# Kernel tuning notes

Hardware: AMD Instinct MI355X
Metric: run time of the kernel (lower is better)

## Reference

```python
import jax, jax.numpy as jnp
import numpy as np

N, E, IN, H, D, C = 30000, 400000, 128, 4, 64, 40
EPS = 1e-5
SLOPE = 0.2  # DGL GATv2Conv leaky_relu negative_slope default


def setup_inputs() -> dict:
    key = jax.random.key(0)
    ks = jax.random.split(key, 20)
    def rn(k, shape, s=0.05):
        return jax.random.normal(k, shape, jnp.float32) * s
    return {
        "x": jax.random.normal(ks[0], (N, IN), jnp.float32),
        "src": jax.random.randint(ks[1], (E,), 0, N),
        "dst": jax.random.randint(ks[2], (E,), 0, N),
        # layer 0: in=128 -> heads*64 (residual projection since 128 != 256)
        "W_src0": rn(ks[3], (IN, H * D)), "W_dst0": rn(ks[4], (IN, H * D)),
        "b0": jnp.zeros((H * D,), jnp.float32), "attn0": rn(ks[5], (H, D)),
        "res_W0": rn(ks[6], (IN, H * D)),
        # layer 1: 256 -> heads*64 (identity residual since 256 == 256)
        "W_src1": rn(ks[7], (H * D, H * D)), "W_dst1": rn(ks[8], (H * D, H * D)),
        "b1": jnp.zeros((H * D,), jnp.float32), "attn1": rn(ks[9], (H, D)),
        # layer 2: 256 -> heads*40 (residual projection)
        "W_src2": rn(ks[10], (H * D, H * C)), "W_dst2": rn(ks[11], (H * D, H * C)),
        "b2": jnp.zeros((H * C,), jnp.float32), "attn2": rn(ks[12], (H, C)),
        "res_W2": rn(ks[13], (H * D, H * C)),
        # batchnorm affine params (training-mode batch stats)
        "g0": jnp.ones((H * D,), jnp.float32), "be0": jnp.zeros((H * D,), jnp.float32),
        "g1": jnp.ones((H * D,), jnp.float32), "be1": jnp.zeros((H * D,), jnp.float32),
    }


def gatv2_layer(h, src, dst, Wsrc, Wdst, b, attn, resW, out_dim, relu_act):
    # DGL GATv2Conv: score_e = attn . leaky_relu(fc_src(h)[u] + fc_dst(h)[v])
    n = h.shape[0]
    fs = (h @ Wsrc).reshape(n, H, out_dim)
    fd = (h @ Wdst).reshape(n, H, out_dim)
    e = jax.nn.leaky_relu(fs[src] + fd[dst], SLOPE)      # [E, H, out]
    score = jnp.einsum("ehd,hd->eh", e, attn)            # [E, H]
    # segment softmax over incoming edges of each dst node
    m = jax.ops.segment_max(score, dst, num_segments=n)
    m = jnp.where(jnp.isfinite(m), m, 0.0)               # zero in-degree safety
    ex = jnp.exp(score - m[dst])
    denom = jax.ops.segment_sum(ex, dst, num_segments=n)
    alpha = ex / jnp.maximum(denom, 1e-9)[dst]
    rst = jax.ops.segment_sum(alpha[:, :, None] * fs[src], dst, num_segments=n)
    res = (h @ resW).reshape(n, H, out_dim) if resW is not None else h.reshape(n, H, out_dim)
    rst = rst + res + b.reshape(1, H, out_dim)
    return jax.nn.relu(rst) if relu_act else rst


def batchnorm(h, g, be):
    mu = h.mean(0)
    var = h.var(0)  # biased variance, as torch BN uses for normalization
    return g * (h - mu) * jax.lax.rsqrt(var + EPS) + be


def reference(x, src, dst, W_src0, W_dst0, b0, attn0, res_W0, W_src1, W_dst1, b1, attn1, W_src2, W_dst2, b2, attn2, res_W2, g0, be0, g1, be1):
    h = gatv2_layer(x, src, dst, W_src0, W_dst0, b0, attn0, res_W0, D, True)
    h = jax.nn.relu(batchnorm(h.reshape(N, H * D), g0, be0))  # dropout = identity (eval)
    h = gatv2_layer(h, src, dst, W_src1, W_dst1, b1, attn1, None, D, True)
    h = jax.nn.relu(batchnorm(h.reshape(N, H * D), g1, be1))
    h = gatv2_layer(h, src, dst, W_src2, W_dst2, b2, attn2, res_W2, C, False)
    h = h.mean(1)  # mean over heads -> [N, C]
    return jax.nn.log_softmax(h, axis=-1)
```

## Files before the change

kernel.cpp:

```cpp
#include <hip/hip_runtime.h>
#include <hip/hip_bf16.h>
#include <math.h>

#define NN 30000
#define EE 400000
#define INP 128
#define HH 4
#define DD 64
#define CC 40
#define HD 256
#define HC 160
#define NBLK 118

typedef unsigned short ushort;
typedef __attribute__((ext_vector_type(8))) short s8v;
typedef __attribute__((ext_vector_type(4))) float f4v;
typedef __attribute__((ext_vector_type(2))) float f2;


__device__ inline ushort bf16_of_float(float f) {
    __hip_bfloat16 b = __float2bfloat16(f);
    return *(ushort*)&b;
}
__device__ __forceinline__ float b2f(ushort u) { return __uint_as_float(((unsigned)u) << 16); }

__device__ __forceinline__ f2 cvt2v(unsigned d) {
    f2 r;
    r.x = __uint_as_float(d << 16);
    r.y = __uint_as_float(d & 0xFFFF0000u);
    return r;
}
__device__ __forceinline__ f2 splat2(float s) { f2 r = {s, s}; return r; }
__device__ __forceinline__ f2 f2fmav(f2 a, f2 b, f2 c) {
#if __has_builtin(__builtin_elementwise_fma)
    return __builtin_elementwise_fma(a, b, c);
#else
    f2 r; r.x = __fmaf_rn(a.x, b.x, c.x); r.y = __fmaf_rn(a.y, b.y, c.y); return r;
#endif
}
__device__ __forceinline__ f2 f2maxv(f2 a, f2 b) {
#if __has_builtin(__builtin_elementwise_max)
    return __builtin_elementwise_max(a, b);
#else
    f2 r; r.x = fmaxf(a.x, b.x); r.y = fmaxf(a.y, b.y); return r;
#endif
}

__device__ __forceinline__ void gld16(const void* g, void* l) {
    __builtin_amdgcn_global_load_lds((const __attribute__((address_space(1))) void*)g,
                                     (__attribute__((address_space(3))) void*)l, 16, 0, 0);
}

__device__ __forceinline__ float rowsum16(float x) {
    int t;
    t = __builtin_amdgcn_update_dpp(0, __float_as_int(x), 0x128, 0xF, 0xF, false); x += __int_as_float(t);
    t = __builtin_amdgcn_update_dpp(0, __float_as_int(x), 0x124, 0xF, 0xF, false); x += __int_as_float(t);
    t = __builtin_amdgcn_update_dpp(0, __float_as_int(x), 0x122, 0xF, 0xF, false); x += __int_as_float(t);
    t = __builtin_amdgcn_update_dpp(0, __float_as_int(x), 0x121, 0xF, 0xF, false); x += __int_as_float(t);
    return x;
}
__device__ __forceinline__ float rowmax16(float x) {
    int t;
    t = __builtin_amdgcn_update_dpp(0, __float_as_int(x), 0x128, 0xF, 0xF, false); x = fmaxf(x, __int_as_float(t));
    t = __builtin_amdgcn_update_dpp(0, __float_as_int(x), 0x124, 0xF, 0xF, false); x = fmaxf(x, __int_as_float(t));
    t = __builtin_amdgcn_update_dpp(0, __float_as_int(x), 0x122, 0xF, 0xF, false); x = fmaxf(x, __int_as_float(t));
    t = __builtin_amdgcn_update_dpp(0, __float_as_int(x), 0x121, 0xF, 0xF, false); x = fmaxf(x, __int_as_float(t));
    return x;
}

#define XB 3750
#define TB 1408
#define ZB 240

__global__ __launch_bounds__(256) void k_prep(const float* __restrict__ x, ushort* __restrict__ xc,
        const float* W0, const float* W1, const float* W2, const float* W3,
        const float* W4, const float* W5, const float* W6, const float* W7,
        ushort* bt0, ushort* bt1, ushort* bt2,
        int* __restrict__ zero_region,
        const float* b0, const float* a0, const float* b1, const float* a1,
        const float* b2, const float* a2, const float* g0, const float* be0,
        const float* g1, const float* be1, ushort* __restrict__ smallv) {
    int b = blockIdx.x, t = threadIdx.x;
    if (b < XB) {
        int i = b * 256 + t;
        if (i < NN * INP / 4) {
            float4 v = ((const float4*)x)[i];
            ushort4 o;
            o.x = bf16_of_float(v.x); o.y = bf16_of_float(v.y);
            o.z = bf16_of_float(v.z); o.w = bf16_of_float(v.w);
            ((ushort4*)xc)[i] = o;
        }
    } else if (b < XB + TB) {
        const float* Ws[8] = {W0, W1, W2, W3, W4, W5, W6, W7};
        int g = (b - XB) * 256 + t;
        if (g < 98304) {
            int seg = g >> 15, local = g & 32767;
            int n = local >> 7, k = local & 127;
            bt0[g] = bf16_of_float(Ws[seg][k * 256 + n]);
        } else if (g < 229376) {
            int gg = g - 98304;
            int seg = gg >> 16, local = gg & 65535;
            int n = local >> 8, k = local & 255;
            bt1[gg] = bf16_of_float(Ws[3 + seg][k * 256 + n]);
        } else if (g < 360448) {
            int gg = g - 229376;
            int n = gg >> 8, k = gg & 255;
            ushort val = 0;
            if (n < 480) {
                int seg = n / 160;
                int nn = n - seg * 160;
                val = bf16_of_float(Ws[5 + seg][k * 160 + nn]);
            }
            bt2[gg] = val;
        }
    } else if (b < XB + TB + ZB) {
        int i = (b - XB - TB) * 256 + t;
        if (i < 1024 + 2 * NN + 192) zero_region[i] = 0;
    } else {
        const float* ptrs[10] = {b0, a0, b1, a1, b2, a2, g0, be0, g1, be1};
        const int sz[10] = {256, 256, 256, 256, 160, 160, 256, 256, 256, 256};
        int off = 0;
        for (int j = 0; j < 10; j++) {
            if (t < sz[j]) smallv[off + t] = bf16_of_float(ptrs[j][t]);
            off += sz[j];
        }
    }
}


__global__ __launch_bounds__(256) void k_hist(const int* __restrict__ dst, int* __restrict__ cnt) {
    int e = blockIdx.x * 256 + threadIdx.x;
    if (e < EE) atomicAdd(&cnt[dst[e]], 1);
}

__global__ __launch_bounds__(256) void k_binbeg(const int* __restrict__ cnt, int* __restrict__ binCnt,
                                                int* __restrict__ beg, int* __restrict__ total) {
    __shared__ int lb[64];
    __shared__ int ss[256];
    __shared__ int base;
    int t = threadIdx.x;
    if (t < 64) lb[t] = 0;
    __syncthreads();
    int i = blockIdx.x * 256 + t;
    int c = (i < NN) ? cnt[i] : 0;
    if (i < NN) atomicAdd(&lb[63 - min(c, 63)], 1);
    ss[t] = c;
    __syncthreads();
    if (t < 64 && lb[t] > 0) atomicAdd(&binCnt[t], lb[t]);
    for (int o = 1; o < 256; o <<= 1) {
        int v = (t >= o) ? ss[t - o] : 0;
        __syncthreads();
        ss[t] += v;
        __syncthreads();
    }
    if (t == 255) base = atomicAdd(total, ss[255]);
    __syncthreads();
    if (i < NN) beg[i] = base + ss[t] - c;
}

__global__ __launch_bounds__(256) void k_orderscatter(const int* __restrict__ cnt, const int* __restrict__ binCnt,
                                                      int* __restrict__ binPos, int* __restrict__ order,
                                                      const int* __restrict__ src, const int* __restrict__ dst,
                                                      const int* __restrict__ beg, int* __restrict__ pos,
                                                      int* __restrict__ srcs) {
    int t = threadIdx.x;
    if (blockIdx.x < NBLK) {
        __shared__ int lb[64], lbase[64], bpre[64];
        if (t < 64) { lb[t] = 0; bpre[t] = binCnt[t]; }
        __syncthreads();
        int i = blockIdx.x * 256 + t;
        int bin = 0, rank = 0;
        if (i < NN) {
            bin = 63 - min(cnt[i], 63);
            rank = atomicAdd(&lb[bin], 1);
        }
        for (int o = 1; o < 64; o <<= 1) {
            int v = (t >= o && t < 64) ? bpre[t - o] : 0;
            __syncthreads();
            if (t < 64) bpre[t] += v;
            __syncthreads();
        }
        if (t < 64 && lb[t] > 0)
            lbase[t] = bpre[t] - binCnt[t] + atomicAdd(&binPos[t], lb[t]);
        __syncthreads();
        if (i < NN) order[lbase[bin] + rank] = i;
    } else {
        int e = (blockIdx.x - NBLK) * 256 + t;
        if (e < EE) {
            int d = dst[e];
            int p = atomicAdd(&pos[d], 1);
            srcs[beg[d] + p] = src[e];
        }
    }
}


template<int K, int SEGW, int NSEG>
__global__ __launch_bounds__(256) void k_gemm_tiled(const ushort* __restrict__ A,
                                                    const ushort* __restrict__ Bt,
                                                    ushort* __restrict__ o0, ushort* __restrict__ o1,
                                                    ushort* __restrict__ o2) {
    __shared__ ushort As[2 * 128 * 32];
    __shared__ ushort Bs[2 * 128 * 32];
    int t = threadIdx.x;
    int wave = t >> 6, lane = t & 63;
    int m = lane & 15, q = lane >> 4;
    int row0 = blockIdx.x * 128, col0 = blockIdx.y * 128;
    int wr = (wave >> 1) << 6, wc = (wave & 1) << 6;
    f4v acc[4][4] = {};
    int c1 = t, c2 = t + 256;
    int ar1 = min(row0 + (c1 >> 2), NN - 1);
    int ar2 = min(row0 + (c2 >> 2), NN - 1);
    const ushort* a1 = A + (size_t)ar1 * K + (c1 & 3) * 8;
    const ushort* a2 = A + (size_t)ar2 * K + (c2 & 3) * 8;
    const ushort* b1 = Bt + (size_t)(col0 + (c1 >> 2)) * K + (c1 & 3) * 8;
    const ushort* b2 = Bt + (size_t)(col0 + (c2 >> 2)) * K + (c2 & 3) * 8;
    int wbase = wave << 10;
    char* AsB = (char*)As;
    char* BsB = (char*)Bs;

    gld16(a1, AsB + wbase);
    gld16(a2, AsB + 4096 + wbase);
    gld16(b1, BsB + wbase);
    gld16(b2, BsB + 4096 + wbase);
    __syncthreads();

#pragma unroll
    for (int kt = 0; kt < K; kt += 32) {
        int cur = (kt >> 5) & 1;
        int curo = cur * 4096;
        if (kt + 32 < K) {
            int nb = (cur ^ 1) * 8192;
            gld16(a1 + kt + 32, AsB + nb + wbase);
            gld16(a2 + kt + 32, AsB + nb + 4096 + wbase);
            gld16(b1 + kt + 32, BsB + nb + wbase);
            gld16(b2 + kt + 32, BsB + nb + 4096 + wbase);
        }
        s8v af[4], bg[4];
#pragma unroll
        for (int i = 0; i < 4; i++) af[i] = *(const s8v*)&As[curo + (wr + i * 16 + m) * 32 + q * 8];
#pragma unroll
        for (int c = 0; c < 4; c++) bg[c] = *(const s8v*)&Bs[curo + (wc + c * 16 + m) * 32 + q * 8];
#pragma unroll
        for (int i = 0; i < 4; i++)
#pragma unroll
            for (int c = 0; c < 4; c++)
                acc[i][c] = __builtin_amdgcn_mfma_f32_16x16x32_bf16(bg[c], af[i], acc[i][c], 0, 0, 0);
        if (kt + 32 < K) __syncthreads();
    }

#pragma unroll
    for (int c = 0; c < 4; c++) {
        int gcb = col0 + wc + c * 16;
        if (gcb < SEGW * NSEG) {
            int seg = gcb / SEGW;
            int colb = gcb - seg * SEGW + q * 4;
            ushort* op = seg == 0 ? o0 : (seg == 1 ? o1 : o2);
#pragma unroll
            for (int i = 0; i < 4; i++) {
                int gr = row0 + wr + i * 16 + m;
                if (gr < NN) {
                    ushort4 s4;
                    s4.x = bf16_of_float(acc[i][c][0]);
                    s4.y = bf16_of_float(acc[i][c][1]);
                    s4.z = bf16_of_float(acc[i][c][2]);
                    s4.w = bf16_of_float(acc[i][c][3]);
                    *(ushort4*)&op[(size_t)gr * SEGW + colb] = s4;
                }
            }
        }
    }
}


template<int DH, bool FINAL>
__global__ __launch_bounds__(256) void k_aggregate(const ushort* __restrict__ fs, const ushort* __restrict__ fd,
                                                   const ushort* __restrict__ res,
                                                   const ushort* __restrict__ attn,
                                                   const ushort* __restrict__ bias,
                                                   const int* __restrict__ beg, const int* __restrict__ cnt,
                                                   const int* __restrict__ srcs,
                                                   const int* __restrict__ order,
                                                   ushort* __restrict__ outb, float* __restrict__ outf) {
    constexpr int F = HH * DH;
    constexpr int JMAX = DH >> 2;
    int tt = threadIdx.x;
    int v = __builtin_amdgcn_readfirstlane(order[blockIdx.x * 4 + (tt >> 6)]);
    int lane = tt & 63;
    int h = lane >> 4, j = lane & 15;
    bool act = j < JMAX;
    unsigned off = h * DH + 4 * j;
    unsigned vbase = (unsigned)v * F + off;
    f2 fda = {0.f, 0.f}, fdb = {0.f, 0.f}, ava = {0.f, 0.f}, avb = {0.f, 0.f};
    if (act) {
        uint2 d = *(const uint2*)&fd[vbase];
        fda = cvt2v(d.x); fdb = cvt2v(d.y);
        uint2 a = *(const uint2*)&attn[off];
        const float LOG2E = 1.4426950408889634f;
        ava = cvt2v(a.x) * LOG2E; avb = cvt2v(a.y) * LOG2E;
    }
    float l = 0.f;
    f2 acca = {0.f, 0.f}, accb = {0.f, 0.f};
    int b0i = beg[v], end = b0i + cnt[v];

    auto ldrow = [&](int u, f2& ra, f2& rb) {
        ra = splat2(0.f); rb = splat2(0.f);
        if (act) {
            uint2 d = *(const uint2*)&fs[(unsigned)u * F + off];
            ra = cvt2v(d.x); rb = cvt2v(d.y);
        }
    };
    auto dotlr = [&](const f2& ra, const f2& rb) -> float {
        f2 t0 = ra + fda;
        f2 t1 = rb + fdb;
        t0 = f2maxv(t0, t0 * 0.2f);
        t1 = f2maxv(t1, t1 * 0.2f);
        f2 p2 = ava * t0;
        p2 = f2fmav(avb, t1, p2);
        return p2.x + p2.y;
    };
    auto quadc = [&](const f2& r0a, const f2& r0b, const f2& r1a, const f2& r1b,
                     const f2& r2a, const f2& r2b, const f2& r3a, const f2& r3b) {
        float p0 = rowsum16(dotlr(r0a, r0b));
        float p1 = rowsum16(dotlr(r1a, r1b));
        float p2 = rowsum16(dotlr(r2a, r2b));
        float p3 = rowsum16(dotlr(r3a, r3b));
        float w0 = exp2f(p0), w1 = exp2f(p1), w2 = exp2f(p2), w3 = exp2f(p3);
        l += (w0 + w1) + (w2 + w3);
        acca = f2fmav(splat2(w0), r0a, acca);
        accb = f2fmav(splat2(w0), r0b, accb);
        acca = f2fmav(splat2(w1), r1a, acca);
        accb = f2fmav(splat2(w1), r1b, accb);
        acca = f2fmav(splat2(w2), r2a, acca);
        accb = f2fmav(splat2(w2), r2b, accb);
        acca = f2fmav(splat2(w3), r3a, acca);
        accb = f2fmav(splat2(w3), r3b, accb);
    };

    int i = b0i;
    if (i + 3 < end) {
        int u0 = srcs[i], u1 = srcs[i+1], u2 = srcs[i+2], u3 = srcs[i+3];
        f2 r0a, r0b, r1a, r1b, r2a, r2b, r3a, r3b;
        ldrow(u0, r0a, r0b); ldrow(u1, r1a, r1b);
        ldrow(u2, r2a, r2b); ldrow(u3, r3a, r3b);
        for (i += 4; i + 3 < end; i += 4) {
            int n0 = srcs[i], n1 = srcs[i+1], n2 = srcs[i+2], n3 = srcs[i+3];
            f2 s0a, s0b, s1a, s1b, s2a, s2b, s3a, s3b;
            ldrow(n0, s0a, s0b); ldrow(n1, s1a, s1b);
            ldrow(n2, s2a, s2b); ldrow(n3, s3a, s3b);
            quadc(r0a, r0b, r1a, r1b, r2a, r2b, r3a, r3b);
            r0a = s0a; r0b = s0b; r1a = s1a; r1b = s1b;
            r2a = s2a; r2b = s2b; r3a = s3a; r3b = s3b;
        }
        quadc(r0a, r0b, r1a, r1b, r2a, r2b, r3a, r3b);
    }
    for (; i < end; i++) {
        f2 ra, rb;
        ldrow(srcs[i], ra, rb);
        float p0 = rowsum16(dotlr(ra, rb));
        float w0 = exp2f(p0);
        l += w0;
        acca = f2fmav(splat2(w0), ra, acca);
        accb = f2fmav(splat2(w0), rb, accb);
    }

    float4 o4 = {0.f, 0.f, 0.f, 0.f};
    if (act) {
        float inv = 1.f / fmaxf(l, 1e-9f);
        uint2 rr = *(const uint2*)&res[vbase];
        f2 rl = cvt2v(rr.x), rh = cvt2v(rr.y);
        uint2 bb = *(const uint2*)&bias[off];
        f2 bl = cvt2v(bb.x), bh = cvt2v(bb.y);
        o4.x = acca.x * inv + rl.x + bl.x;
        o4.y = acca.y * inv + rl.y + bl.y;
        o4.z = accb.x * inv + rh.x + bh.x;
        o4.w = accb.y * inv + rh.y + bh.y;
        if (!FINAL) {
            o4.x = fmaxf(o4.x, 0.f); o4.y = fmaxf(o4.y, 0.f);
            o4.z = fmaxf(o4.z, 0.f); o4.w = fmaxf(o4.w, 0.f);
        }
    }
    if (!FINAL) {
        if (act) {
            ushort4 s4;
            s4.x = bf16_of_float(o4.x); s4.y = bf16_of_float(o4.y);
            s4.z = bf16_of_float(o4.z); s4.w = bf16_of_float(o4.w);
            *(ushort4*)&outb[vbase] = s4;
        }
    } else {
#pragma unroll
        for (int msk = 16; msk <= 32; msk <<= 1) {
            o4.x += __shfl_xor(o4.x, msk, 64);
            o4.y += __shfl_xor(o4.y, msk, 64);
            o4.z += __shfl_xor(o4.z, msk, 64);
            o4.w += __shfl_xor(o4.w, msk, 64);
        }
        float4 zv = make_float4(0.25f * o4.x, 0.25f * o4.y, 0.25f * o4.z, 0.25f * o4.w);
        float mx4 = act ? fmaxf(fmaxf(zv.x, zv.y), fmaxf(zv.z, zv.w)) : -1e30f;
        float mx = rowmax16(mx4);
        float es = 0.f;
        if (act) es = __expf(zv.x - mx) + __expf(zv.y - mx) + __expf(zv.z - mx) + __expf(zv.w - mx);
        float ssum = rowsum16(es);
        float lse = mx + logf(ssum);
        if (act && h == 0) {
            float4 w4 = make_float4(zv.x - lse, zv.y - lse, zv.z - lse, zv.w - lse);
            *(float4*)&outf[(size_t)v * CC + 4 * j] = w4;
        }
    }
}


__global__ __launch_bounds__(256) void k_bn_partial(const ushort* __restrict__ h, float* __restrict__ sum,
                                                    float* __restrict__ sumsq) {
    int c = threadIdx.x;
    int r0 = blockIdx.x * 128;
    int r1 = min(NN, r0 + 128);
    float s0 = 0.f, ss0 = 0.f, s1 = 0.f, ss1 = 0.f;
    int r = r0;
#pragma unroll 4
    for (; r + 1 < r1; r += 2) {
        float v0 = b2f(h[(size_t)r * HD + c]);
        float v1 = b2f(h[(size_t)(r + 1) * HD + c]);
        s0 += v0; ss0 = __fmaf_rn(v0, v0, ss0);
        s1 += v1; ss1 = __fmaf_rn(v1, v1, ss1);
    }
    if (r < r1) {
        float v0 = b2f(h[(size_t)r * HD + c]);
        s0 += v0; ss0 = __fmaf_rn(v0, v0, ss0);
    }
    atomicAdd(&sum[c], s0 + s1);
    atomicAdd(&sumsq[c], ss0 + ss1);
}


__global__ __launch_bounds__(256) void k_bn_norm(const ushort* __restrict__ hin, const float* __restrict__ sum,
                                                 const float* __restrict__ sumsq,
                                                 const ushort* __restrict__ g,
                                                 const ushort* __restrict__ be,
                                                 ushort* __restrict__ hbf) {
    int i4 = blockIdx.x * 256 + threadIdx.x;
    if (i4 < NN * HD / 4) {
        int base = i4 * 4;
        int c = base & (HD - 1);
        ushort4 hv = ((const ushort4*)hin)[i4];
        ushort4 ov;
        float vv[4] = {b2f(hv.x), b2f(hv.y), b2f(hv.z), b2f(hv.w)};
        ushort* po = (ushort*)&ov;
#pragma unroll
        for (int k = 0; k < 4; k++) {
            float mean = sum[c + k] * (1.0f / NN);
            float var = fmaxf(sumsq[c + k] * (1.0f / NN) - mean * mean, 0.f);
            float y = b2f(g[c + k]) * (vv[k] - mean) * rsqrtf(var + 1e-5f) + b2f(be[c + k]);
            po[k] = bf16_of_float(fmaxf(y, 0.f));
        }
        ((ushort4*)hbf)[i4] = ov;
    }
}


static inline char* alignup(char* p) { return (char*)(((size_t)p + 255) & ~(size_t)255); }

extern "C" void kernel_launch(void* const* d_in, const int* in_sizes, int n_in,
                              void* d_out, int out_size, void* d_ws, size_t ws_size,
                              hipStream_t stream) {
    const float* x     = (const float*)d_in[0];
    const int*  src    = (const int*)d_in[1];
    const int*  dst    = (const int*)d_in[2];
    const float* Wsrc0 = (const float*)d_in[3];
    const float* Wdst0 = (const float*)d_in[4];
    const float* b0    = (const float*)d_in[5];
    const float* attn0 = (const float*)d_in[6];
    const float* resW0 = (const float*)d_in[7];
    const float* Wsrc1 = (const float*)d_in[8];
    const float* Wdst1 = (const float*)d_in[9];
    const float* b1    = (const float*)d_in[10];
    const float* attn1 = (const float*)d_in[11];
    const float* Wsrc2 = (const float*)d_in[12];
    const float* Wdst2 = (const float*)d_in[13];
    const float* b2    = (const float*)d_in[14];
    const float* attn2 = (const float*)d_in[15];
    const float* resW2 = (const float*)d_in[16];
    const float* g0    = (const float*)d_in[17];
    const float* be0   = (const float*)d_in[18];
    const float* g1    = (const float*)d_in[19];
    const float* be1   = (const float*)d_in[20];

    char* w = (char*)d_ws;
    const size_t NF = (size_t)NN * HD;
    ushort* fsb = (ushort*)w; w += NF * 2;
    ushort* fdb = (ushort*)w; w += NF * 2;
    ushort* resb= (ushort*)w; w += NF * 2;
    ushort* hag = (ushort*)w; w += NF * 2;
    ushort* hbf = (ushort*)w; w += NF * 2;
    ushort* xc  = (ushort*)w; w += (size_t)NN * INP * 2;
    ushort* bt0 = (ushort*)w; w += 768 * 128 * 2;
    ushort* bt1 = (ushort*)w; w += 512 * 256 * 2;
    ushort* bt2 = (ushort*)w; w += 512 * 256 * 2;
    ushort* smallv = (ushort*)w; w += 2368 * 2; w = alignup(w);
    float* bnstats = (float*)w; w += 1024 * 4;
    int* cnt    = (int*)w; w += NN * 4;
    int* pos    = (int*)w; w += NN * 4;
    int* binCnt = (int*)w; w += 64 * 4;
    int* binPos = (int*)w; w += 64 * 4;
    int* total  = (int*)w; w += 64 * 4; w = alignup(w);
    int* beg    = (int*)w; w += NN * 4; w = alignup(w);
    int* order  = (int*)w; w += NN * 4; w = alignup(w);
    int* srcs   = (int*)w; w += EE * 4;

    const ushort* c_b0    = smallv + 0;
    const ushort* c_attn0 = smallv + 256;
    const ushort* c_b1    = smallv + 512;
    const ushort* c_attn1 = smallv + 768;
    const ushort* c_b2    = smallv + 1024;
    const ushort* c_attn2 = smallv + 1184;
    const ushort* c_g0    = smallv + 1344;
    const ushort* c_be0   = smallv + 1600;
    const ushort* c_g1    = smallv + 1856;
    const ushort* c_be1   = smallv + 2112;

    k_prep<<<XB + TB + ZB + 1, 256, 0, stream>>>(x, xc,
        Wsrc0, Wdst0, resW0, Wsrc1, Wdst1, Wsrc2, Wdst2, resW2, bt0, bt1, bt2,
        (int*)bnstats,
        b0, attn0, b1, attn1, b2, attn2, g0, be0, g1, be1, smallv);

    k_hist<<<(EE + 255) / 256, 256, 0, stream>>>(dst, cnt);
    k_binbeg<<<NBLK, 256, 0, stream>>>(cnt, binCnt, beg, total);
    k_orderscatter<<<NBLK + (EE + 255) / 256, 256, 0, stream>>>(cnt, binCnt, binPos, order,
                                                                src, dst, beg, pos, srcs);

    const int MB = (NN + 127) / 128;

    k_gemm_tiled<128, 256, 3><<<dim3(MB, 6), 256, 0, stream>>>(xc, bt0, fsb, fdb, resb);
    k_aggregate<DD, false><<<NN / 4, 256, 0, stream>>>(fsb, fdb, resb, c_attn0, c_b0,
        beg, cnt, srcs, order, hag, nullptr);
    k_bn_partial<<<MB, 256, 0, stream>>>(hag, bnstats, bnstats + 256);
    k_bn_norm<<<(int)((NF / 4 + 255) / 256), 256, 0, stream>>>(hag, bnstats, bnstats + 256,
                                                               c_g0, c_be0, hbf);

    k_gemm_tiled<256, 256, 2><<<dim3(MB, 4), 256, 0, stream>>>(hbf, bt1, fsb, fdb, nullptr);
    k_aggregate<DD, false><<<NN / 4, 256, 0, stream>>>(fsb, fdb, hbf, c_attn1, c_b1,
        beg, cnt, srcs, order, hag, nullptr);
    k_bn_partial<<<MB, 256, 0, stream>>>(hag, bnstats + 512, bnstats + 768);
    k_bn_norm<<<(int)((NF / 4 + 255) / 256), 256, 0, stream>>>(hag, bnstats + 512, bnstats + 768,
                                                               c_g1, c_be1, hbf);

    k_gemm_tiled<256, 160, 3><<<dim3(MB, 4), 256, 0, stream>>>(hbf, bt2, fsb, fdb, resb);
    k_aggregate<CC, true><<<NN / 4, 256, 0, stream>>>(fsb, fdb, resb, c_attn2, c_b2,
        beg, cnt, srcs, order, nullptr, (float*)d_out);
}
```

Before: 361.4 us.

## Pad CSR segments to 4, vectorize source index loads, single-buffer GEMM LDS

Each node's CSR segment is rounded up to a multiple of four edges, so segment starts are 16-byte aligned. The aggregation loop can then fetch four source indices with one int4 load and prefetch the next group one iteration ahead, with a sched barrier to keep the loads ahead of the compute. The GEMM drops its double-buffered LDS staging for a single buffer with two barriers per k-step, which halves shared memory per block and may raise occupancy. The cost is losing load/compute overlap in the GEMM and a larger srcs buffer.

```diff
diff --git a/kernel.cpp b/kernel.cpp
--- a/kernel.cpp
+++ b/kernel.cpp
@@ -143,8 +143,9 @@
     __syncthreads();
     int i = blockIdx.x * 256 + t;
     int c = (i < NN) ? cnt[i] : 0;
+    int rc = (c + 3) & ~3;
     if (i < NN) atomicAdd(&lb[63 - min(c, 63)], 1);
-    ss[t] = c;
+    ss[t] = rc;
     __syncthreads();
     if (t < 64 && lb[t] > 0) atomicAdd(&binCnt[t], lb[t]);
     for (int o = 1; o < 256; o <<= 1) {
@@ -155,7 +156,7 @@
     }
     if (t == 255) base = atomicAdd(total, ss[255]);
     __syncthreads();
-    if (i < NN) beg[i] = base + ss[t] - c;
+    if (i < NN) beg[i] = base + ss[t] - rc;
 }
 
 __global__ __launch_bounds__(256) void k_orderscatter(const int* __restrict__ cnt, const int* __restrict__ binCnt,
@@ -200,8 +201,8 @@
                                                     const ushort* __restrict__ Bt,
                                                     ushort* __restrict__ o0, ushort* __restrict__ o1,
                                                     ushort* __restrict__ o2) {
-    __shared__ ushort As[2 * 128 * 32];
-    __shared__ ushort Bs[2 * 128 * 32];
+    __shared__ ushort As[128 * 32];
+    __shared__ ushort Bs[128 * 32];
     int t = threadIdx.x;
     int wave = t >> 6, lane = t & 63;
     int m = lane & 15, q = lane >> 4;
@@ -219,34 +220,24 @@
     char* AsB = (char*)As;
     char* BsB = (char*)Bs;
 
-    gld16(a1, AsB + wbase);
-    gld16(a2, AsB + 4096 + wbase);
-    gld16(b1, BsB + wbase);
-    gld16(b2, BsB + 4096 + wbase);
-    __syncthreads();
-
 #pragma unroll
     for (int kt = 0; kt < K; kt += 32) {
-        int cur = (kt >> 5) & 1;
-        int curo = cur * 4096;
-        if (kt + 32 < K) {
-            int nb = (cur ^ 1) * 8192;
-            gld16(a1 + kt + 32, AsB + nb + wbase);
-            gld16(a2 + kt + 32, AsB + nb + 4096 + wbase);
-            gld16(b1 + kt + 32, BsB + nb + wbase);
-            gld16(b2 + kt + 32, BsB + nb + 4096 + wbase);
-        }
+        __syncthreads();
+        gld16(a1 + kt, AsB + wbase);
+        gld16(a2 + kt, AsB + 4096 + wbase);
+        gld16(b1 + kt, BsB + wbase);
+        gld16(b2 + kt, BsB + 4096 + wbase);
+        __syncthreads();
         s8v af[4], bg[4];
 #pragma unroll
-        for (int i = 0; i < 4; i++) af[i] = *(const s8v*)&As[curo + (wr + i * 16 + m) * 32 + q * 8];
-#pragma unroll
-        for (int c = 0; c < 4; c++) bg[c] = *(const s8v*)&Bs[curo + (wc + c * 16 + m) * 32 + q * 8];
+        for (int i = 0; i < 4; i++) af[i] = *(const s8v*)&As[(wr + i * 16 + m) * 32 + q * 8];
+#pragma unroll
+        for (int c = 0; c < 4; c++) bg[c] = *(const s8v*)&Bs[(wc + c * 16 + m) * 32 + q * 8];
 #pragma unroll
         for (int i = 0; i < 4; i++)
 #pragma unroll
             for (int c = 0; c < 4; c++)
                 acc[i][c] = __builtin_amdgcn_mfma_f32_16x16x32_bf16(bg[c], af[i], acc[i][c], 0, 0, 0);
-        if (kt + 32 < K) __syncthreads();
     }
 
 #pragma unroll
@@ -339,15 +330,17 @@
 
     int i = b0i;
     if (i + 3 < end) {
-        int u0 = srcs[i], u1 = srcs[i+1], u2 = srcs[i+2], u3 = srcs[i+3];
+        int4 u = *(const int4*)&srcs[i];
         f2 r0a, r0b, r1a, r1b, r2a, r2b, r3a, r3b;
-        ldrow(u0, r0a, r0b); ldrow(u1, r1a, r1b);
-        ldrow(u2, r2a, r2b); ldrow(u3, r3a, r3b);
+        ldrow(u.x, r0a, r0b); ldrow(u.y, r1a, r1b);
+        ldrow(u.z, r2a, r2b); ldrow(u.w, r3a, r3b);
+        int4 un = (i + 7 < end) ? *(const int4*)&srcs[i + 4] : u;
         for (i += 4; i + 3 < end; i += 4) {
-            int n0 = srcs[i], n1 = srcs[i+1], n2 = srcs[i+2], n3 = srcs[i+3];
             f2 s0a, s0b, s1a, s1b, s2a, s2b, s3a, s3b;
-            ldrow(n0, s0a, s0b); ldrow(n1, s1a, s1b);
-            ldrow(n2, s2a, s2b); ldrow(n3, s3a, s3b);
+            ldrow(un.x, s0a, s0b); ldrow(un.y, s1a, s1b);
+            ldrow(un.z, s2a, s2b); ldrow(un.w, s3a, s3b);
+            if (i + 7 < end) un = *(const int4*)&srcs[i + 4];
+            __builtin_amdgcn_sched_barrier(0);
             quadc(r0a, r0b, r1a, r1b, r2a, r2b, r3a, r3b);
             r0a = s0a; r0b = s0b; r1a = s1a; r1b = s1b;
             r2a = s2a; r2b = s2b; r3a = s3a; r3b = s3b;
@@ -505,7 +498,7 @@
     int* total  = (int*)w; w += 64 * 4; w = alignup(w);
     int* beg    = (int*)w; w += NN * 4; w = alignup(w);
     int* order  = (int*)w; w += NN * 4; w = alignup(w);
-    int* srcs   = (int*)w; w += EE * 4;
+    int* srcs   = (int*)w; w += (size_t)(EE + 3 * NN + 64) * 4;
 
     const ushort* c_b0    = smallv + 0;
     const ushort* c_attn0 = smallv + 256;
```

Result: no change. 361.2 us (-0.1%).
